# Performance work log

Measured on AMD Instinct MI355X. Metric: run time of the kernel, lower is better.

## Reference

```python
import jax, jax.numpy as jnp
import numpy as np

B, K, D = 65536, 1024, 256
COMMITMENT_COST = 0.25


def setup_inputs() -> dict:
    key = jax.random.key(0)
    kz, kw = jax.random.split(key)
    z = jax.random.normal(kz, (B, D), dtype=jnp.float32)
    # torch init: uniform_(-1/num_embeddings, 1/num_embeddings)
    weight = jax.random.uniform(kw, (K, D), dtype=jnp.float32,
                                minval=-1.0 / K, maxval=1.0 / K)
    return {"z": z, "weight": weight}


def reference(z, weight):
    # squared L2 distances via expansion: ||z||^2 - 2 z.e + ||e||^2  -> [B, K]
    dists = (jnp.sum(z * z, axis=1, keepdims=True)
             - 2.0 * (z @ weight.T)
             + jnp.sum(weight * weight, axis=1))
    indices = jnp.argmin(dists, axis=1)          # [B]
    z_q = weight[indices]                         # [B, D] gather

    sg_z = jax.lax.stop_gradient(z)
    mse = jnp.mean((z_q - sg_z) ** 2)
    commitment_loss = COMMITMENT_COST * mse      # F.mse_loss(z.detach(), z_q)
    vq_loss = mse + commitment_loss              # F.mse_loss(z_q, z.detach()) + commitment

    # straight-through estimator
    z_q_st = z + jax.lax.stop_gradient(z_q - z)
    return z_q_st, vq_loss, indices
```

## Files before the change

### kernel.cpp

```cpp
#include <hip/hip_runtime.h>
#include <math.h>

#define B_N 65536
#define K_N 1024
#define D_N 256
#define CAPW 512
#define NWV 8

typedef __attribute__((ext_vector_type(8))) short bf16x8;
typedef __attribute__((ext_vector_type(4))) float f32x4;

__device__ __forceinline__ unsigned short f2bf(float f) {
    unsigned u = __float_as_uint(f);
    return (unsigned short)((u + 0x7FFFu + ((u >> 16) & 1u)) >> 16);
}
__device__ __forceinline__ unsigned encf(float f) {
    unsigned u = __float_as_uint(f);
    return u ^ ((unsigned)((int)u >> 31) | 0x80000000u);
}
__device__ __forceinline__ float decf(unsigned e) {
    unsigned u = (e & 0x80000000u) ? (e ^ 0x80000000u) : ~e;
    return __uint_as_float(u);
}
__device__ __forceinline__ void gload_lds16(const void* g, void* l) {
    __builtin_amdgcn_global_load_lds(
        (const __attribute__((address_space(1))) unsigned int*)g,
        (__attribute__((address_space(3))) unsigned int*)l, 16, 0, 0);
}

__device__ __forceinline__ float chain_dot(const float* __restrict__ zp,
                                           const float* __restrict__ wp) {
    float acc = 0.0f;
    #pragma unroll 1
    for (int j = 0; j < 64; ++j) {
        float4 za = *reinterpret_cast<const float4*>(zp + (j << 2));
        float4 wa = *reinterpret_cast<const float4*>(wp + (j << 2));
        acc = fmaf(za.x, wa.x, acc);
        acc = fmaf(za.y, wa.y, acc);
        acc = fmaf(za.z, wa.z, acc);
        acc = fmaf(za.w, wa.w, acc);
    }
    return acc;
}

__device__ __forceinline__ int pA(int i, int k) {
    return ((i + k) & 15) - 7 + 9 * ((k >> 4) & 1);
}
__device__ __forceinline__ int pB(int j, int k) {
    return ((j + 3 * k) & 15) - 7 + 5 * ((k >> 4) & 1);
}

__global__ void mfma_probe_kernel(int* __restrict__ flag) {
    const int l = threadIdx.x & 63;
    const int c15 = l & 15, g = l >> 4;
    bf16x8 afr[8], bfr[8];
    #pragma unroll
    for (int m = 0; m < 8; ++m)
        #pragma unroll
        for (int e = 0; e < 8; ++e) {
            const int k = m * 32 + g * 8 + e;
            afr[m][e] = (short)f2bf((float)pA(c15, k));
            bfr[m][e] = (short)f2bf((float)pB(c15, k));
        }
    f32x4 acc = {0.f, 0.f, 0.f, 0.f};
    #pragma unroll
    for (int m = 0; m < 8; ++m)
        acc = __builtin_amdgcn_mfma_f32_16x16x32_bf16(afr[m], bfr[m], acc, 0, 0, 0);
    int h1 = 1, h2 = 1;
    #pragma unroll 1
    for (int reg = 0; reg < 4; ++reg) {
        const int q = 4 * g + reg;
        int e1 = 0, e2 = 0;
        for (int k = 0; k < 32; ++k) {
            e1 += pA(q, k) * pB(c15, k);
            e2 += pA(c15, k) * pB(q, k);
        }
        e1 *= 8; e2 *= 8;
        if (acc[reg] != (float)e1) h1 = 0;
        if (acc[reg] != (float)e2) h2 = 0;
    }
    h1 = __all(h1); h2 = __all(h2);
    if (threadIdx.x == 0) *flag = h1 ? 0 : (h2 ? 1 : 2);
}

__global__ void wprep_kernel(const float* __restrict__ w,
                             float* __restrict__ ww,
                             unsigned short* __restrict__ wb) {
    int wave = (int)((blockIdx.x * blockDim.x + threadIdx.x) >> 6);
    int lane = threadIdx.x & 63;
    if (wave >= K_N) return;
    const float4 v = *reinterpret_cast<const float4*>(w + ((size_t)wave << 8) + (lane << 2));
    float s = v.x * v.x + v.y * v.y + v.z * v.z + v.w * v.w;
    #pragma unroll
    for (int off = 32; off; off >>= 1) s += __shfl_xor(s, off, 64);
    if (lane == 0) ww[wave] = s;
    ushort4 b;
    b.x = f2bf(v.x); b.y = f2bf(v.y); b.z = f2bf(v.z); b.w = f2bf(v.w);
    const int mp = lane >> 3;
    const int gp = (lane >> 1) & 3;
    const int hp = (wave >> 4) & 1;
    const size_t off_b = (size_t)(wave >> 5) * 16384
        + (size_t)(((hp * 8 + mp) * 64 + gp * 16 + (wave & 15)) * 16)
        + (size_t)((lane & 1) * 8);
    *reinterpret_cast<ushort4*>((char*)wb + off_b) = b;
}

__global__ __launch_bounds__(512, 4)
void vq_mfma_kernel(const float* __restrict__ z, const float* __restrict__ w,
                    const unsigned short* __restrict__ wb,
                    const float* __restrict__ ww,
                    const int* __restrict__ flagp,
                    float* __restrict__ zq_out,
                    float* __restrict__ idxf_out,
                    double* __restrict__ partial) {
    __shared__ alignas(16) short wbl[2][8192];
    __shared__ float wwlds[1024];
    __shared__ unsigned short rc[NWV][CAPW];
    __shared__ unsigned short dqv[NWV][CAPW];
    __shared__ float zz_l[NWV][16], band_l[NWV][16], thrm[NWV][16];
    __shared__ unsigned rowminU[NWV][16];
    __shared__ unsigned long long bestk[NWV][16];

    const int tid = threadIdx.x;
    const int wv = tid >> 6, l = tid & 63;
    const int c15 = l & 15, g = l >> 4;
    const int b0 = blockIdx.x << 7;
    const int rbase = b0 + (wv << 4);
    const int flag = flagp[0];
    const bool fb0 = !(flag == 0 || flag == 1);

#define STAGE(T, BUF) do {                                                    \
        const char* _s = (const char*)wb + (size_t)(T) * 16384 + tid * 16;    \
        char* _d = (char*)&wbl[BUF][0] + tid * 16;                            \
        gload_lds16(_s,         _d);                                          \
        gload_lds16(_s + 8192,  _d + 8192);                                   \
    } while (0)

    STAGE(0, 0);

    if (l < 16) {
        rowminU[wv][l] = 0xFFFFFFFFu;
        bestk[wv][l]   = ~0ull;
    }
    reinterpret_cast<float2*>(wwlds)[tid] = reinterpret_cast<const float2*>(ww)[tid];

    #pragma unroll 1
    for (int r = 0; r < 16; ++r) {
        const float4 v = *reinterpret_cast<const float4*>(
            z + ((size_t)(rbase + r) << 8) + (l << 2));
        float s = v.x * v.x + v.y * v.y + v.z * v.z + v.w * v.w;
        float a = fabsf(v.x) + fabsf(v.y) + fabsf(v.z) + fabsf(v.w);
        #pragma unroll
        for (int off = 32; off; off >>= 1) {
            s += __shfl_xor(s, off, 64);
            a += __shfl_xor(a, off, 64);
        }
        if (l == 0) {
            zz_l[wv][r]   = s;
            band_l[wv][r] = a * 2.0e-5f + 1.0e-3f;
        }
    }

    bool fbw = fb0;
    int n = 0;

    int ml[4], cl[4];
    #pragma unroll
    for (int reg = 0; reg < 4; ++reg) {
        if (flag == 1) { ml[reg] = c15;          cl[reg] = 4 * g + reg; }
        else           { ml[reg] = 4 * g + reg;  cl[reg] = c15;         }
    }
    float zzv[4], bdv[4];
    #pragma unroll
    for (int reg = 0; reg < 4; ++reg) {
        zzv[reg] = zz_l[wv][ml[reg]];
        bdv[reg] = band_l[wv][ml[reg]];
    }

    bf16x8 afr[8];
    {
        const float* zr = z + ((size_t)(rbase + c15) << 8) + (g << 3);
        #pragma unroll
        for (int m = 0; m < 8; ++m) {
            float4 lo = *reinterpret_cast<const float4*>(zr + (m << 5));
            float4 hi = *reinterpret_cast<const float4*>(zr + (m << 5) + 4);
            bf16x8 f;
            f[0] = (short)f2bf(lo.x); f[1] = (short)f2bf(lo.y);
            f[2] = (short)f2bf(lo.z); f[3] = (short)f2bf(lo.w);
            f[4] = (short)f2bf(hi.x); f[5] = (short)f2bf(hi.y);
            f[6] = (short)f2bf(hi.z); f[7] = (short)f2bf(hi.w);
            afr[m] = f;
        }
    }

    __syncthreads();

    float runmin[4] = {INFINITY, INFINITY, INFINITY, INFINITY};
    int base = 0;

    if (!fb0) {
        #pragma unroll 1
        for (int t = 0; t < 32; ++t) {
            if (t < 31) STAGE(t + 1, (t + 1) & 1);

            const short* sb = wbl[t & 1];
            #pragma unroll
            for (int h = 0; h < 2; ++h) {
                f32x4 acc = {0.f, 0.f, 0.f, 0.f};
                #pragma unroll
                for (int m = 0; m < 8; ++m) {
                    bf16x8 bfr = *reinterpret_cast<const bf16x8*>(
                        &sb[((h * 8 + m) << 9) + (l << 3)]);
                    acc = __builtin_amdgcn_mfma_f32_16x16x32_bf16(afr[m], bfr, acc, 0, 0, 0);
                }
                #pragma unroll
                for (int reg = 0; reg < 4; ++reg) {
                    const int code = (t << 5) + (h << 4) + cl[reg];
                    const float dist = (zzv[reg] - 2.0f * acc[reg]) + wwlds[code];
                    if (t > 0) {
                        const bool pred = (dist <= runmin[reg] + bdv[reg]);
                        const unsigned long long mask = __ballot(pred);
                        if (pred) {
                            const int slot = base + (int)__popcll(mask & ((1ull << l) - 1ull));
                            if (slot < CAPW) {
                                rc[wv][slot] = (unsigned short)((ml[reg] << 10) | code);
                                union { _Float16 h16; unsigned short u; } cv;
                                cv.h16 = (_Float16)(dist - zzv[reg]);
                                dqv[wv][slot] = cv.u;
                            }
                        }
                        base += (int)__popcll(mask);
                    }
                    runmin[reg] = fminf(runmin[reg], dist);
                }
            }

            if (flag == 1) {
                #pragma unroll
                for (int reg = 0; reg < 4; ++reg) {
                    runmin[reg] = fminf(runmin[reg], __shfl_xor(runmin[reg], 16, 64));
                    runmin[reg] = fminf(runmin[reg], __shfl_xor(runmin[reg], 32, 64));
                }
            } else {
                #pragma unroll
                for (int reg = 0; reg < 4; ++reg) {
                    runmin[reg] = fminf(runmin[reg], __shfl_xor(runmin[reg], 1, 64));
                    runmin[reg] = fminf(runmin[reg], __shfl_xor(runmin[reg], 2, 64));
                    runmin[reg] = fminf(runmin[reg], __shfl_xor(runmin[reg], 4, 64));
                    runmin[reg] = fminf(runmin[reg], __shfl_xor(runmin[reg], 8, 64));
                }
            }
            __syncthreads();
        }

        STAGE(0, 0);
        __syncthreads();
        {
            const short* sb = wbl[0];
            #pragma unroll
            for (int h = 0; h < 2; ++h) {
                f32x4 acc = {0.f, 0.f, 0.f, 0.f};
                #pragma unroll
                for (int m = 0; m < 8; ++m) {
                    bf16x8 bfr = *reinterpret_cast<const bf16x8*>(
                        &sb[((h * 8 + m) << 9) + (l << 3)]);
                    acc = __builtin_amdgcn_mfma_f32_16x16x32_bf16(afr[m], bfr, acc, 0, 0, 0);
                }
                #pragma unroll
                for (int reg = 0; reg < 4; ++reg) {
                    const int code = (h << 4) + cl[reg];
                    const float dist = (zzv[reg] - 2.0f * acc[reg]) + wwlds[code];
                    const bool pred = (dist <= runmin[reg] + bdv[reg]);
                    const unsigned long long mask = __ballot(pred);
                    if (pred) {
                        const int slot = base + (int)__popcll(mask & ((1ull << l) - 1ull));
                        if (slot < CAPW) {
                            rc[wv][slot] = (unsigned short)((ml[reg] << 10) | code);
                            union { _Float16 h16; unsigned short u; } cv;
                            cv.h16 = (_Float16)(dist - zzv[reg]);
                            dqv[wv][slot] = cv.u;
                        }
                    }
                    base += (int)__popcll(mask);
                }
            }
        }

        n = base;
        if (n > CAPW) fbw = true;

        #pragma unroll
        for (int reg = 0; reg < 4; ++reg)
            atomicMin(&rowminU[wv][ml[reg]], encf(runmin[reg]));
        if (l < 16)
            thrm[wv][l] = (decf(rowminU[wv][l]) + band_l[wv][l]) - zz_l[wv][l] + 4.0e-4f;
    }
#undef STAGE

    if (!fbw) {
        int viol = 0;
        #pragma unroll 1
        for (int i = l; i < n; i += 64) {
            const int e = rc[wv][i];
            const int m = e >> 10, code = e & 1023;
            union { _Float16 h16; unsigned short u; } cv;
            cv.u = dqv[wv][i];
            const float dval = (float)cv.h16;
            if (dval <= thrm[wv][m]) {
                const float dot = chain_dot(z + ((size_t)(rbase + m) << 8),
                                            w + ((size_t)code << 8));
                const float dist = (zz_l[wv][m] - 2.0f * dot) + wwlds[code];
                if (fabsf((dval + zz_l[wv][m]) - dist) > band_l[wv][m] + 4.0e-4f)
                    viol = 1;
                atomicMin(&bestk[wv][m],
                          ((unsigned long long)encf(dist) << 32) | (unsigned)code);
            }
        }
        if (__any(viol)) fbw = true;
    }
    if (fbw) {
        #pragma unroll 1
        for (int m = 0; m < 16; ++m) {
            const float zzm = zz_l[wv][m];
            const float* zp = z + ((size_t)(rbase + m) << 8);
            for (int code = l; code < 1024; code += 64) {
                const float dist = (zzm - 2.0f * chain_dot(zp, w + ((size_t)code << 8)))
                                 + wwlds[code];
                atomicMin(&bestk[wv][m],
                          ((unsigned long long)encf(dist) << 32) | (unsigned)code);
            }
        }
    }

    if (l < 16) {
        const int code = (int)(unsigned)(bestk[wv][l] & 0xFFFFFFFFull);
        idxf_out[rbase + l] = (float)code;
    }

    double s = 0.0;
    #pragma unroll 1
    for (int rr = 0; rr < 16; ++rr) {
        const int code = (int)(unsigned)(bestk[wv][rr] & 0xFFFFFFFFull);
        const float4 wv4 = *reinterpret_cast<const float4*>(
            w + ((size_t)code << 8) + (l << 2));
        const float4 zv4 = *reinterpret_cast<const float4*>(
            z + ((size_t)(rbase + rr) << 8) + (l << 2));
        *reinterpret_cast<float4*>(
            zq_out + ((size_t)(rbase + rr) << 8) + (l << 2)) = wv4;
        const float dx = wv4.x - zv4.x, dy = wv4.y - zv4.y;
        const float dz = wv4.z - zv4.z, dw = wv4.w - zv4.w;
        s += (double)dx * dx + (double)dy * dy + (double)dz * dz + (double)dw * dw;
    }
    __syncthreads();
    double* sd = reinterpret_cast<double*>(&wbl[0][0]);
    sd[tid] = s;
    __syncthreads();
    #pragma unroll
    for (int off = 256; off; off >>= 1) {
        if (tid < off) sd[tid] += sd[tid + off];
        __syncthreads();
    }
    if (tid == 0) partial[blockIdx.x] = sd[0];
}

__global__ void finalize_loss_kernel(const double* __restrict__ partial,
                                     float* __restrict__ out) {
    __shared__ double sd[256];
    const int t = threadIdx.x;
    double s = 0.0;
    for (int i = t; i < 512; i += 256) s += partial[i];
    sd[t] = s;
    __syncthreads();
    #pragma unroll
    for (int off = 128; off; off >>= 1) {
        if (t < off) sd[t] += sd[t + off];
        __syncthreads();
    }
    if (t == 0) {
        double mse = sd[0] / ((double)B_N * (double)D_N);
        out[0] = (float)(mse * 1.25);
    }
}

extern "C" void kernel_launch(void* const* d_in, const int* in_sizes, int n_in,
                              void* d_out, int out_size, void* d_ws, size_t ws_size,
                              hipStream_t stream) {
    const float* z = (const float*)d_in[0];
    const float* w = (const float*)d_in[1];

    float* out  = (float*)d_out;
    float* zq   = out;
    float* loss = out + (size_t)B_N * D_N;
    float* idxf = loss + 1;

    char* wsb = (char*)d_ws;
    float*          ww      = (float*)(wsb);
    unsigned short* wb      = (unsigned short*)(wsb + 4096);
    int*            flag    = (int*)(wsb + 528384);
    double*         partial = (double*)(wsb + 528448);

    mfma_probe_kernel<<<1, 64, 0, stream>>>(flag);

    wprep_kernel<<<K_N / 4, 256, 0, stream>>>(w, ww, wb);

    vq_mfma_kernel<<<B_N / 128, 512, 0, stream>>>(z, w, wb, ww, flag,
                                                  zq, idxf, partial);

    finalize_loss_kernel<<<1, 256, 0, stream>>>(partial, loss);
}
```

Baseline: 179.8 us.

## Triple-buffer codebook staging with counted waits and fold rescan into main loop

Moves the codebook LDS staging from double to triple buffering, prefetching two tiles ahead and using explicit s_waitcnt vmcnt counts plus a raw s_barrier in place of __syncthreads. The separate rescan pass of tile 0 becomes a 33rd iteration of the main loop. The z-norm loads are batched eight rows at a time, and the final gather loop reads its codes into registers up front and unrolls by two. The aim is to hide global-to-LDS latency and cut barrier stalls. In exchange, LDS use per block grows by 16 KB, which may lower occupancy under launch_bounds(512,4), and the hand-written waitcnt counts must match the number of outstanding loads.

```diff
diff --git a/kernel.cpp b/kernel.cpp
--- a/kernel.cpp
+++ b/kernel.cpp
@@ -113,7 +113,7 @@
                     float* __restrict__ zq_out,
                     float* __restrict__ idxf_out,
                     double* __restrict__ partial) {
-    __shared__ alignas(16) short wbl[2][8192];
+    __shared__ alignas(16) short wbl[3][8192];
     __shared__ float wwlds[1024];
     __shared__ unsigned short rc[NWV][CAPW];
     __shared__ unsigned short dqv[NWV][CAPW];
@@ -145,21 +145,30 @@
     reinterpret_cast<float2*>(wwlds)[tid] = reinterpret_cast<const float2*>(ww)[tid];
 
     #pragma unroll 1
-    for (int r = 0; r < 16; ++r) {
-        const float4 v = *reinterpret_cast<const float4*>(
-            z + ((size_t)(rbase + r) << 8) + (l << 2));
-        float s = v.x * v.x + v.y * v.y + v.z * v.z + v.w * v.w;
-        float a = fabsf(v.x) + fabsf(v.y) + fabsf(v.z) + fabsf(v.w);
+    for (int half = 0; half < 2; ++half) {
+        float4 vrow[8];
         #pragma unroll
-        for (int off = 32; off; off >>= 1) {
-            s += __shfl_xor(s, off, 64);
-            a += __shfl_xor(a, off, 64);
-        }
-        if (l == 0) {
-            zz_l[wv][r]   = s;
-            band_l[wv][r] = a * 2.0e-5f + 1.0e-3f;
-        }
-    }
+        for (int r = 0; r < 8; ++r)
+            vrow[r] = *reinterpret_cast<const float4*>(
+                z + ((size_t)(rbase + half * 8 + r) << 8) + (l << 2));
+        #pragma unroll
+        for (int r = 0; r < 8; ++r) {
+            const float4 v = vrow[r];
+            float s = v.x * v.x + v.y * v.y + v.z * v.z + v.w * v.w;
+            float a = fabsf(v.x) + fabsf(v.y) + fabsf(v.z) + fabsf(v.w);
+            #pragma unroll
+            for (int off = 32; off; off >>= 1) {
+                s += __shfl_xor(s, off, 64);
+                a += __shfl_xor(a, off, 64);
+            }
+            if (l == 0) {
+                zz_l[wv][half * 8 + r]   = s;
+                band_l[wv][half * 8 + r] = a * 2.0e-5f + 1.0e-3f;
+            }
+        }
+    }
+
+    STAGE(1, 1);
 
     bool fbw = fb0;
     int n = 0;
@@ -169,12 +178,6 @@
     for (int reg = 0; reg < 4; ++reg) {
         if (flag == 1) { ml[reg] = c15;          cl[reg] = 4 * g + reg; }
         else           { ml[reg] = 4 * g + reg;  cl[reg] = c15;         }
-    }
-    float zzv[4], bdv[4];
-    #pragma unroll
-    for (int reg = 0; reg < 4; ++reg) {
-        zzv[reg] = zz_l[wv][ml[reg]];
-        bdv[reg] = band_l[wv][ml[reg]];
     }
 
     bf16x8 afr[8];
@@ -195,15 +198,26 @@
 
     __syncthreads();
 
+    float zzv[4], bdv[4];
+    #pragma unroll
+    for (int reg = 0; reg < 4; ++reg) {
+        zzv[reg] = zz_l[wv][ml[reg]];
+        bdv[reg] = band_l[wv][ml[reg]];
+    }
+
     float runmin[4] = {INFINITY, INFINITY, INFINITY, INFINITY};
     int base = 0;
 
     if (!fb0) {
         #pragma unroll 1
-        for (int t = 0; t < 32; ++t) {
-            if (t < 31) STAGE(t + 1, (t + 1) & 1);
-
-            const short* sb = wbl[t & 1];
+        for (int t = 0; t <= 32; ++t) {
+            if (t + 2 <= 32) {
+                const int st = (t + 2 <= 31) ? (t + 2) : 0;
+                STAGE(st, (t + 2) % 3);
+            }
+
+            const short* sb = wbl[t % 3];
+            const int tc = (t <= 31) ? t : 0;
             #pragma unroll
             for (int h = 0; h < 2; ++h) {
                 f32x4 acc = {0.f, 0.f, 0.f, 0.f};
@@ -215,7 +229,7 @@
                 }
                 #pragma unroll
                 for (int reg = 0; reg < 4; ++reg) {
-                    const int code = (t << 5) + (h << 4) + cl[reg];
+                    const int code = (tc << 5) + (h << 4) + cl[reg];
                     const float dist = (zzv[reg] - 2.0f * acc[reg]) + wwlds[code];
                     if (t > 0) {
                         const bool pred = (dist <= runmin[reg] + bdv[reg]);
@@ -231,58 +245,34 @@
                         }
                         base += (int)__popcll(mask);
                     }
-                    runmin[reg] = fminf(runmin[reg], dist);
+                    if (t < 32) runmin[reg] = fminf(runmin[reg], dist);
                 }
             }
 
-            if (flag == 1) {
-                #pragma unroll
-                for (int reg = 0; reg < 4; ++reg) {
-                    runmin[reg] = fminf(runmin[reg], __shfl_xor(runmin[reg], 16, 64));
-                    runmin[reg] = fminf(runmin[reg], __shfl_xor(runmin[reg], 32, 64));
+            if (t < 32) {
+                if (flag == 1) {
+                    #pragma unroll
+                    for (int reg = 0; reg < 4; ++reg) {
+                        runmin[reg] = fminf(runmin[reg], __shfl_xor(runmin[reg], 16, 64));
+                        runmin[reg] = fminf(runmin[reg], __shfl_xor(runmin[reg], 32, 64));
+                    }
+                } else {
+                    #pragma unroll
+                    for (int reg = 0; reg < 4; ++reg) {
+                        runmin[reg] = fminf(runmin[reg], __shfl_xor(runmin[reg], 1, 64));
+                        runmin[reg] = fminf(runmin[reg], __shfl_xor(runmin[reg], 2, 64));
+                        runmin[reg] = fminf(runmin[reg], __shfl_xor(runmin[reg], 4, 64));
+                        runmin[reg] = fminf(runmin[reg], __shfl_xor(runmin[reg], 8, 64));
+                    }
                 }
-            } else {
-                #pragma unroll
-                for (int reg = 0; reg < 4; ++reg) {
-                    runmin[reg] = fminf(runmin[reg], __shfl_xor(runmin[reg], 1, 64));
-                    runmin[reg] = fminf(runmin[reg], __shfl_xor(runmin[reg], 2, 64));
-                    runmin[reg] = fminf(runmin[reg], __shfl_xor(runmin[reg], 4, 64));
-                    runmin[reg] = fminf(runmin[reg], __shfl_xor(runmin[reg], 8, 64));
+                if (t + 2 <= 32) {
+                    asm volatile("s_waitcnt vmcnt(2) lgkmcnt(0)" ::: "memory");
+                } else {
+                    asm volatile("s_waitcnt vmcnt(0) lgkmcnt(0)" ::: "memory");
                 }
-            }
-            __syncthreads();
-        }
-
-        STAGE(0, 0);
-        __syncthreads();
-        {
-            const short* sb = wbl[0];
-            #pragma unroll
-            for (int h = 0; h < 2; ++h) {
-                f32x4 acc = {0.f, 0.f, 0.f, 0.f};
-                #pragma unroll
-                for (int m = 0; m < 8; ++m) {
-                    bf16x8 bfr = *reinterpret_cast<const bf16x8*>(
-                        &sb[((h * 8 + m) << 9) + (l << 3)]);
-                    acc = __builtin_amdgcn_mfma_f32_16x16x32_bf16(afr[m], bfr, acc, 0, 0, 0);
-                }
-                #pragma unroll
-                for (int reg = 0; reg < 4; ++reg) {
-                    const int code = (h << 4) + cl[reg];
-                    const float dist = (zzv[reg] - 2.0f * acc[reg]) + wwlds[code];
-                    const bool pred = (dist <= runmin[reg] + bdv[reg]);
-                    const unsigned long long mask = __ballot(pred);
-                    if (pred) {
-                        const int slot = base + (int)__popcll(mask & ((1ull << l) - 1ull));
-                        if (slot < CAPW) {
-                            rc[wv][slot] = (unsigned short)((ml[reg] << 10) | code);
-                            union { _Float16 h16; unsigned short u; } cv;
-                            cv.h16 = (_Float16)(dist - zzv[reg]);
-                            dqv[wv][slot] = cv.u;
-                        }
-                    }
-                    base += (int)__popcll(mask);
-                }
+                __builtin_amdgcn_sched_barrier(0);
+                __builtin_amdgcn_s_barrier();
+                __builtin_amdgcn_sched_barrier(0);
             }
         }
 
@@ -337,10 +327,14 @@
         idxf_out[rbase + l] = (float)code;
     }
 
+    int codes[16];
+    #pragma unroll
+    for (int rr = 0; rr < 16; ++rr)
+        codes[rr] = (int)(unsigned)(bestk[wv][rr] & 0xFFFFFFFFull);
     double s = 0.0;
-    #pragma unroll 1
+    #pragma unroll 2
     for (int rr = 0; rr < 16; ++rr) {
-        const int code = (int)(unsigned)(bestk[wv][rr] & 0xFFFFFFFFull);
+        const int code = codes[rr];
         const float4 wv4 = *reinterpret_cast<const float4*>(
             w + ((size_t)code << 8) + (l << 2));
         const float4 zv4 = *reinterpret_cast<const float4*>(
```

New measurement: 178.5 us. About the same (-0.7%).
